# Kernel optimization log

Hardware: AMD Instinct MI355X
Metric: run time of the kernel (lower is better)

Reference implementation:

```python
import jax, jax.numpy as jnp
import numpy as np

BS, L, ED = 4, 2048, 1024
D = ED // 2          # time_embedding_dim = 512
ANG_HID = D // 4     # AngleEmb hidden = 128
T_MAX = 1010


def _gelu(x):
    return jax.nn.gelu(x, approximate=False)  # torch F.gelu default = exact erf


def _time_embed(t, w1, b1, w2, b2):
    # sinusoidal (diffusion-style, base 10000) + 2-layer MLP; t: [N] float
    half = D // 2
    freqs = jnp.exp(-jnp.log(10000.0) * jnp.arange(half, dtype=jnp.float32) / half)
    a = t[:, None] * freqs[None, :]
    e = jnp.concatenate([jnp.sin(a), jnp.cos(a)], axis=-1)  # [N, D]
    return _gelu(e @ w1 + b1) @ w2 + b2


def _cal_dist(p, aa_seq):
    # p: [bs, L, 3]; ragged per-segment mean pairwise distance.
    # Segments run (cls_idx+1 .. eos_idx-1]; token 0 = cls, token 2 = eos.
    cls = (aa_seq == 0)
    eos = (aa_seq == 2)
    seg = jnp.cumsum(cls.astype(jnp.int32), axis=1)                       # segment id
    valid = (seg > jnp.cumsum(eos.astype(jnp.int32), axis=1)) & ~cls & ~eos
    same = (seg[:, :, None] == seg[:, None, :]) & valid[:, :, None] & valid[:, None, :]
    diff = p[:, :, None, :] - p[:, None, :, :]                            # [bs,L,L,3]
    sq = jnp.sum(diff * diff, axis=-1)
    d = jnp.where(sq > 0, jnp.sqrt(jnp.where(sq > 0, sq, 1.0)), 0.0)      # safe norm
    cnt = jnp.sum(same, axis=-1)                                           # segment size (incl self)
    dist = jnp.where(valid, jnp.sum(d * same, axis=-1) / jnp.maximum(cnt, 1), 0.0)
    return dist[..., None]                                                 # [bs,L,1]


def setup_inputs() -> dict:
    key = jax.random.key(0)
    ks = jax.random.split(key, 26)
    # build ragged aa_seq: repeated [cls=0, residues in [3,25), eos=2], pad token 1
    rng = np.random.default_rng(0)
    aa = np.ones((BS, L), dtype=np.int64)
    pad = np.ones((BS, L), dtype=bool)
    for b in range(BS):
        i = 0
        while i < L - 8:
            seg = int(rng.integers(16, 64))
            seg = min(seg, L - i - 2)
            aa[b, i] = 0
            aa[b, i + 1:i + 1 + seg] = rng.integers(3, 25, size=seg)
            aa[b, i + 1 + seg] = 2
            pad[b, i:i + 2 + seg] = False
            i += seg + 2
    s = 0.05
    inp = {
        "pos": jax.random.normal(ks[0], (BS, L, 3, 3), jnp.float32) * 5.0,
        "angle": jax.random.uniform(ks[1], (BS, L, 6), jnp.float32, -3.14, 3.14),
        "padding_mask": jnp.asarray(pad),
        "mask_aa": jax.random.bernoulli(ks[2], 0.15, (BS, L, 1)),
        "mask_pos": jax.random.bernoulli(ks[3], 0.15, (BS, L, 1)),
        "mask_angle": jax.random.bernoulli(ks[4], 0.15, (BS, L, 1)),
        "angle_mask": jax.random.bernoulli(ks[5], 0.9, (BS, L, 3)),
        "bond_angle_mask": jax.random.bernoulli(ks[6], 0.9, (BS, L, 3)),
        "time_pos": jax.random.randint(ks[7], (BS, L), 0, T_MAX).astype(jnp.float32),
        "time_angle": jnp.zeros((BS, L, 6), jnp.float32),  # overwritten in fwd (dim-2 path)
        "aa_seq": jnp.asarray(aa),
        # parameters ([in, out] layout; torch Linear bias=False unless noted)
        "ang_w1": jax.random.normal(ks[8], (1, ANG_HID), jnp.float32) * 0.5,
        "ang_w2": jax.random.normal(ks[9], (ANG_HID, D), jnp.float32) * s,
        "pos_w1": jax.random.normal(ks[10], (1, 1), jnp.float32) * 0.5,
        "pos_w2": jax.random.normal(ks[11], (1, D), jnp.float32) * s,
        "te_w1": jax.random.normal(ks[12], (D, D), jnp.float32) * s,
        "te_b1": jnp.zeros((D,), jnp.float32),
        "te_w2": jax.random.normal(ks[13], (D, D), jnp.float32) * s,
        "te_b2": jnp.zeros((D,), jnp.float32),
        "angproj_w": jax.random.normal(ks[14], (6 * D, D), jnp.float32) * s,
        "angproj_b": jnp.zeros((D,), jnp.float32),
        "posproj_w": jax.random.normal(ks[15], (D, D), jnp.float32) * s,
        "posproj_b": jnp.zeros((D,), jnp.float32),
        "cls_w": jax.random.normal(ks[16], (1, ED), jnp.float32) * s,
        "eos_w": jax.random.normal(ks[17], (1, ED), jnp.float32) * s,
        "unkang_w": jax.random.normal(ks[18], (1, D), jnp.float32) * s,
        "unkpos_w": jax.random.normal(ks[19], (1, D), jnp.float32) * s,
    }
    return inp


def reference(pos, angle, padding_mask, mask_aa, mask_pos, mask_angle,
              angle_mask, bond_angle_mask, time_pos, time_angle, aa_seq,
              ang_w1, ang_w2, pos_w1, pos_w2,
              te_w1, te_b1, te_w2, te_b2,
              angproj_w, angproj_b, posproj_w, posproj_b,
              cls_w, eos_w, unkang_w, unkpos_w):
    bs, nnode, _ = angle.shape
    amask = jnp.concatenate([angle_mask[:, :, :3], bond_angle_mask], axis=-1)  # [bs,L,6]
    ang = jnp.where(amask, angle, 0.0).reshape(bs, -1, 1)                      # [bs,6L,1]
    cls_mask = (aa_seq == 0)[..., None]
    eos_mask = (aa_seq == 2)[..., None]

    angle_feat = _gelu(ang @ ang_w1) @ ang_w2                                  # [bs,6L,D]
    angle_feat = jnp.where(amask.reshape(bs, -1, 1), angle_feat, unkang_w[0])

    dist = _cal_dist(pos[:, :, 1, :], aa_seq)                                  # [bs,L,1]
    pos_feat = _gelu(dist @ pos_w1) @ pos_w2                                   # [bs,L,D]
    pos_mask = ~(cls_mask | eos_mask)
    pos_feat = jnp.where(pos_mask, pos_feat, unkpos_w[0])

    # time_pos is 2-D -> [bs,L,1]; time_angle := time_pos repeated to [bs,L,6]
    ta = jnp.where(amask, jnp.broadcast_to(time_pos[..., None], (bs, nnode, 6)), 0.0)
    temb_pos = _time_embed(time_pos.reshape(-1), te_w1, te_b1, te_w2, te_b2).reshape(bs, -1, D)
    temb_ang = _time_embed(ta.reshape(-1), te_w1, te_b1, te_w2, te_b2).reshape(bs, -1, D)
    t0_emb = _time_embed(jnp.zeros((1,), jnp.float32), te_w1, te_b1, te_w2, te_b2)[0]  # all-zero t rows are identical

    t_mask = mask_angle & ~cls_mask & ~eos_mask                                # [bs,L,1]
    temb_ang = jnp.where(jnp.tile(t_mask, (1, 6, 1)), temb_ang, t0_emb)        # torch .repeat(1,6,1)
    temb_pos = jnp.where(t_mask, temb_pos, t0_emb)
    angle_feat = angle_feat + temb_ang
    pos_feat = pos_feat + temb_pos

    angle_feat = angle_feat.reshape(bs, nnode, 6 * D) @ angproj_w + angproj_b  # [bs,L,D]
    pos_feat = pos_feat @ posproj_w + posproj_b                                # [bs,L,D]
    node = jnp.concatenate([angle_feat, pos_feat], axis=-1)                    # [bs,L,ED]
    node = jnp.where(cls_mask, cls_w[0], node)
    node = jnp.where(eos_mask, eos_w[0], node)
    node = jnp.where(padding_mask[..., None], 0.0, node)
    return node
```

## Files before the change

### kernel.cpp

```cpp
#include <hip/hip_runtime.h>
#include <hip/hip_bf16.h>
#include <cstdint>
#include <cstddef>

#define BSZ 4
#define SEQL 2048
#define DDIM 512
#define AHID 128
#define NROWS (BSZ*SEQL)
#define NANG (NROWS*6)
#define KCAT 768
#define NTT 1024

typedef __attribute__((ext_vector_type(8))) short short8;
typedef __attribute__((ext_vector_type(4))) float f32x4;
typedef __hip_bfloat16 bf16;

__device__ __forceinline__ float gelu_f(float x){
  return 0.5f * x * (1.0f + erff(x * 0.7071067811865475f));
}

__device__ __forceinline__ void gload16(const void* g, void* l){
  __builtin_amdgcn_global_load_lds(
      (const __attribute__((address_space(1))) unsigned int*)g,
      (__attribute__((address_space(3))) unsigned int*)l,
      16, 0, 0);
}

__device__ __forceinline__ unsigned int packbf2(float a, float b){
  __hip_bfloat16 ha = __float2bfloat16(a), hb = __float2bfloat16(b);
  return (unsigned int)(*(unsigned short*)&ha) | ((unsigned int)(*(unsigned short*)&hb) << 16);
}

#define NB_SCAN 4
#define NB_ANGH 3072
#define NB_SIN  256
#define NB_TR   2208
#define NB_PREP 32
#define NB_MV   224
#define NB_TOTAL (NB_SCAN+NB_ANGH+NB_SIN+NB_TR+NB_PREP+NB_MV)

__device__ void do_transpose(const float* __restrict__ W, bf16* __restrict__ Wt,
                             int K, int q, float (*tsh)[33]){
  int k0 = (q >> 4)*32, n0 = (q & 15)*32;
  int tx = threadIdx.x & 31, ty = threadIdx.x >> 5;
  #pragma unroll
  for (int i=0;i<32;i+=8)
    tsh[ty+i][tx] = W[(size_t)(k0+ty+i)*512 + n0+tx];
  __syncthreads();
  #pragma unroll
  for (int i=0;i<32;i+=8)
    Wt[(size_t)(n0+ty+i)*K + k0+tx] = __float2bfloat16(tsh[tx][ty+i]);
}

__global__ void prologue_kernel(const float* __restrict__ angle,
                                const int* __restrict__ angm, const int* __restrict__ bondm,
                                const int* __restrict__ mask_angle, const int* __restrict__ aa,
                                const int* __restrict__ padm,
                                const float* __restrict__ pos,
                                const float* __restrict__ ang_w1,
                                const float* __restrict__ te_w1, const float* __restrict__ te_w2,
                                const float* __restrict__ te_b2,
                                const float* __restrict__ ang_w2, const float* __restrict__ angproj_w,
                                const float* __restrict__ posproj_w,
                                const float* __restrict__ unkang, const float* __restrict__ pos_w2,
                                float4* __restrict__ pk,
                                bf16* __restrict__ Hang, bf16* __restrict__ et,
                                bf16* __restrict__ tw1t, bf16* __restrict__ apjt,
                                bf16* __restrict__ ppjt, bf16* __restrict__ w2b,
                                bf16* __restrict__ tw2b,
                                unsigned char* __restrict__ amb, unsigned char* __restrict__ scb,
                                float* __restrict__ U, float* __restrict__ Wg,
                                float* __restrict__ qb){
  __shared__ float tsh[32][33];
  __shared__ int wcs[4], wes[4];
  int blk = blockIdx.x;
  int tid = threadIdx.x;
  if (blk < NB_SCAN){
    int b = blk;
    int base = b*SEQL + tid*8;
    int av[8];
    int lc=0, le=0;
    #pragma unroll
    for (int i=0;i<8;i++){ int a=aa[base+i]; av[i]=a; lc += (a==0); le += (a==2); }
    int lane = tid & 63, wid = tid >> 6;
    int pc=lc, pe=le;
    #pragma unroll
    for (int off=1; off<64; off<<=1){
      int tc = __shfl_up(pc, off);
      int te = __shfl_up(pe, off);
      if (lane >= off){ pc += tc; pe += te; }
    }
    if (lane == 63){ wcs[wid] = pc; wes[wid] = pe; }
    __syncthreads();
    int c = pc - lc, eo = pe - le;
    for (int w2=0; w2<wid; w2++){ c += wcs[w2]; eo += wes[w2]; }
    #pragma unroll
    for (int i=0;i<8;i++){
      int a = av[i];
      c += (a==0); eo += (a==2);
      bool valid = (c>eo) && (a!=0) && (a!=2);
      float4 q;
      q.x = pos[(size_t)(base+i)*9+3];
      q.y = pos[(size_t)(base+i)*9+4];
      q.z = pos[(size_t)(base+i)*9+5];
      q.w = valid ? (float)c : -1.f;
      pk[base+i] = q;
    }
    return;
  }
  blk -= NB_SCAN;
  if (blk < NB_ANGH){
    int gidx = blk*256 + tid;
    int row = gidx >> 4;
    int kb = (gidx & 15) * 8;
    int bq = row / (SEQL*6);
    int rr = row - bq*(SEQL*6);
    int l = rr / 6, j = rr - l*6;
    int bl = bq*SEQL + l;
    int m = (j<3) ? angm[bl*3+j] : bondm[bl*3+(j-3)];
    float x = m ? angle[bl*6+j] : 0.f;
    float4 w0 = *(const float4*)(ang_w1+kb);
    float4 w1v = *(const float4*)(ang_w1+kb+4);
    uint4 st;
    st.x = packbf2(gelu_f(x*w0.x),  gelu_f(x*w0.y));
    st.y = packbf2(gelu_f(x*w0.z),  gelu_f(x*w0.w));
    st.z = packbf2(gelu_f(x*w1v.x), gelu_f(x*w1v.y));
    st.w = packbf2(gelu_f(x*w1v.z), gelu_f(x*w1v.w));
    *(uint4*)(Hang + (size_t)row*AHID + kb) = st;
    return;
  }
  blk -= NB_ANGH;
  if (blk < NB_SIN){
    int gidx = blk*256 + tid;
    int row = gidx >> 6;
    int db = (gidx & 63) * 8;
    float t = (float)row;
    float v[8];
    #pragma unroll
    for (int i=0;i<8;i++){
      int d = db + i;
      int k = d & 255;
      float f = exp2f(-0.05190512648262f * (float)k);
      float a = t * f;
      v[i] = (d < 256) ? __sinf(a) : __cosf(a);
    }
    uint4 st;
    st.x = packbf2(v[0],v[1]); st.y = packbf2(v[2],v[3]);
    st.z = packbf2(v[4],v[5]); st.w = packbf2(v[6],v[7]);
    *(uint4*)(et + (size_t)row*DDIM + db) = st;
    return;
  }
  blk -= NB_SIN;
  if (blk < NB_TR){
    if (blk < 256)       do_transpose(te_w1, tw1t, 512, blk, tsh);
    else if (blk < 1792) do_transpose(angproj_w, apjt, 3072, blk-256, tsh);
    else if (blk < 2048) do_transpose(posproj_w, ppjt, 512, blk-1792, tsh);
    else if (blk < 2080){
      int gidx = (blk-2048)*256 + tid;
      float4 a0 = *(const float4*)(ang_w2 + (size_t)gidx*8);
      float4 a1 = *(const float4*)(ang_w2 + (size_t)gidx*8 + 4);
      uint4 st;
      st.x = packbf2(a0.x,a0.y); st.y = packbf2(a0.z,a0.w);
      st.z = packbf2(a1.x,a1.y); st.w = packbf2(a1.z,a1.w);
      *(uint4*)(w2b + (size_t)gidx*8) = st;
    } else {
      int gidx = (blk-2080)*256 + tid;
      float4 a0 = *(const float4*)(te_w2 + (size_t)gidx*8);
      float4 a1 = *(const float4*)(te_w2 + (size_t)gidx*8 + 4);
      uint4 st;
      st.x = packbf2(a0.x,a0.y); st.y = packbf2(a0.z,a0.w);
      st.z = packbf2(a1.x,a1.y); st.w = packbf2(a1.z,a1.w);
      *(uint4*)(tw2b + (size_t)gidx*8) = st;
    }
    return;
  }
  blk -= NB_TR;
  if (blk < NB_PREP){
    int bl = blk*256 + tid;
    int b = bl >> 11, l = bl & (SEQL-1);
    int a = aa[bl];
    bool rowOK = (a!=0) && (a!=2) && (padm[bl]==0);
    int ab=0, sb=0;
    #pragma unroll
    for (int j=0;j<6;j++){
      int am = (j<3) ? angm[bl*3+j] : bondm[bl*3+(j-3)];
      int rr = l*6 + j;
      int bl2 = b*SEQL + (rr & (SEQL-1));
      int a2 = aa[bl2];
      bool tm = mask_angle[bl2] && (a2!=0) && (a2!=2);
      bool qs = tm && (am!=0) && rowOK;
      if (am)  ab |= (1<<j);
      if (qs)  sb |= (1<<j);
    }
    if ((mask_angle[bl]!=0) && rowOK) sb |= 64;
    amb[bl] = (unsigned char)ab;
    scb[bl] = (unsigned char)sb;
    return;
  }
  blk -= NB_PREP;
  {
    int q = blk;
    if (q < 96){
      int j = q >> 4, rem = q & 15;
      int nc = rem >> 3, dc = rem & 7;
      int n = nc*256 + tid, d0 = dc*64;
      float s = 0.f;
      #pragma unroll 4
      for (int i=0;i<64;i++)
        s += unkang[d0+i] * angproj_w[((size_t)(j*512 + d0+i))*512 + n];
      atomicAdd(U + j*512 + n, s);
      return;
    }
    q -= 96;
    if (q < 16){
      int nc = q >> 3, dc = q & 7;
      int n = nc*256 + tid, d0 = dc*64;
      float s = 0.f;
      #pragma unroll 4
      for (int i=0;i<64;i++)
        s += pos_w2[d0+i] * posproj_w[(size_t)(d0+i)*512 + n];
      atomicAdd(Wg + n, s);
      return;
    }
    q -= 16;
    {
      int j = q >> 4, rem = q & 15;
      int nc = rem >> 3, dc = rem & 7;
      int n = nc*256 + tid, d0 = dc*64;
      const float* W = (j<6) ? (angproj_w + (size_t)(j*512)*512) : posproj_w;
      float s = 0.f;
      #pragma unroll 4
      for (int i=0;i<64;i++)
        s += te_b2[d0+i] * W[(size_t)(d0+i)*512 + n];
      atomicAdd(qb + j*512 + n, s);
    }
  }
}

struct EpiArgs {
  const float* bias;
  const unsigned char* amb;
  const unsigned char* scb;
  const float* U;
  const float* Y;
  const float* tp;
  const int* aa;
  const int* pad;
  const float* cls;
  const float* eos;
  float* outF;
  bf16* outB;
  int cnt;
  int coloff;
  int ldc;
};

#define STG_BYTES 12288
#define SMEM_BYTES 49152

template<int EPI>
__device__ __forceinline__ void gemm_core(const char* gA, const char* gB,
                                          int K, int bm, int bn, const EpiArgs& ea, char* smem){
  const int tid = threadIdx.x;
  const int w = tid >> 6, lane = tid & 63;
  const bool doB = (w < 4);
  const int wm = (w>>1)*32, wn = (w&1)*32;
  const int lm = lane & 15, kq = lane >> 4;
  const int sw = kq ^ ((lm>>1)&3);
  const int NT = K >> 5;

  f32x4 acc[2][2];
  #pragma unroll
  for (int i=0;i<2;i++)
    #pragma unroll
    for (int j=0;j<2;j++) acc[i][j] = (f32x4){0.f,0.f,0.f,0.f};

  #pragma unroll
  for (int s=0; s<3; ++s){
    char* base = smem + s*STG_BYTES;
    gload16(gA + (size_t)s*64, base + w*1024);
    if (doB) gload16(gB + (size_t)s*64, base + 8192 + w*1024);
  }

  for (int t = 0; t < NT; ++t){
    char* cur = smem + (t&3)*STG_BYTES;
    if (t+3 < NT){
      char* nxt = smem + ((t+3)&3)*STG_BYTES;
      gload16(gA + (size_t)(t+3)*64, nxt + w*1024);
      if (doB) gload16(gB + (size_t)(t+3)*64, nxt + 8192 + w*1024);
    }
    int ia = NT-1-t; if (ia > 3) ia = 3;
    if (doB){
      if      (ia==3) __asm__ volatile("s_waitcnt vmcnt(6)" ::: "memory");
      else if (ia==2) __asm__ volatile("s_waitcnt vmcnt(4)" ::: "memory");
      else if (ia==1) __asm__ volatile("s_waitcnt vmcnt(2)" ::: "memory");
      else            __asm__ volatile("s_waitcnt vmcnt(0)" ::: "memory");
    } else {
      if      (ia==3) __asm__ volatile("s_waitcnt vmcnt(3)" ::: "memory");
      else if (ia==2) __asm__ volatile("s_waitcnt vmcnt(2)" ::: "memory");
      else if (ia==1) __asm__ volatile("s_waitcnt vmcnt(1)" ::: "memory");
      else            __asm__ volatile("s_waitcnt vmcnt(0)" ::: "memory");
    }
    __builtin_amdgcn_s_barrier();
    short8 af[2], bfr[2];
    #pragma unroll
    for (int tt=0;tt<2;tt++) af[tt]  = *(const short8*)(cur + (wm+tt*16+lm)*64 + sw*16);
    #pragma unroll
    for (int tt=0;tt<2;tt++) bfr[tt] = *(const short8*)(cur + 8192 + (wn+tt*16+lm)*64 + sw*16);
    #pragma unroll
    for (int mt=0;mt<2;mt++)
      #pragma unroll
      for (int nt=0;nt<2;nt++)
        acc[mt][nt] = __builtin_amdgcn_mfma_f32_16x16x32_bf16(af[mt], bfr[nt], acc[mt][nt], 0, 0, 0);
    __builtin_amdgcn_s_barrier();
  }

  float* eps = (float*)smem + w*576;
  const int erow = lane >> 2;
  const int ecg  = (lane & 3) * 8;
  #pragma unroll
  for (int mt=0; mt<2; mt++){
    #pragma unroll
    for (int nt=0; nt<2; nt++)
      #pragma unroll
      for (int rr=0; rr<4; rr++)
        eps[(kq*4+rr)*36 + nt*16 + lm] = acc[mt][nt][rr];
    __asm__ volatile("s_waitcnt lgkmcnt(0)" ::: "memory");
    float4 t0v = *(float4*)(eps + erow*36 + ecg);
    float4 t1v = *(float4*)(eps + erow*36 + ecg + 4);
    float v[8] = {t0v.x,t0v.y,t0v.z,t0v.w,t1v.x,t1v.y,t1v.z,t1v.w};
    __asm__ volatile("s_waitcnt lgkmcnt(0)" ::: "memory");
    int row = bm + wm + mt*16 + erow;
    int col = bn + wn + ecg;

    if (EPI==0 || EPI==1){
      float4 b0 = *(const float4*)(ea.bias+col), b1 = *(const float4*)(ea.bias+col+4);
      float bb[8] = {b0.x,b0.y,b0.z,b0.w,b1.x,b1.y,b1.z,b1.w};
      #pragma unroll
      for (int i=0;i<8;i++){
        v[i] += bb[i];
        if (EPI==0) v[i] = gelu_f(v[i]);
      }
      uint4 st;
      st.x = packbf2(v[0],v[1]); st.y = packbf2(v[2],v[3]);
      st.z = packbf2(v[4],v[5]); st.w = packbf2(v[6],v[7]);
      *(uint4*)(ea.outB + (size_t)row*ea.ldc + col) = st;
    } else if (EPI==4){
      uint4 st;
      st.x = packbf2(v[0],v[1]); st.y = packbf2(v[2],v[3]);
      st.z = packbf2(v[4],v[5]); st.w = packbf2(v[6],v[7]);
      *(uint4*)(ea.outB + (size_t)row*ea.ldc + col + ea.coloff) = st;
    } else if (EPI==5){
      float4 b0 = *(const float4*)(ea.bias+col), b1 = *(const float4*)(ea.bias+col+4);
      v[0]+=b0.x; v[1]+=b0.y; v[2]+=b0.z; v[3]+=b0.w;
      v[4]+=b1.x; v[5]+=b1.y; v[6]+=b1.z; v[7]+=b1.w;
      int ab = ea.amb[row], sc = ea.scb[row];
      int trow = (int)ea.tp[row];
      #pragma unroll
      for (int j=0;j<6;j++){
        float mU = ((ab>>j)&1) ? 0.f : 1.f;
        const float* Up = ea.U + j*512 + col;
        float4 u0=*(const float4*)Up, u1=*(const float4*)(Up+4);
        int idx = ((sc>>j)&1) ? trow : 0;
        const float* yp = ea.Y + ((size_t)j*NTT + idx)*512 + col;
        float4 y0=*(const float4*)yp, y1=*(const float4*)(yp+4);
        v[0]+=mU*u0.x+y0.x; v[1]+=mU*u0.y+y0.y;
        v[2]+=mU*u0.z+y0.z; v[3]+=mU*u0.w+y0.w;
        v[4]+=mU*u1.x+y1.x; v[5]+=mU*u1.y+y1.y;
        v[6]+=mU*u1.z+y1.z; v[7]+=mU*u1.w+y1.w;
      }
      int a = ea.aa[row];
      if (a==0){
        float4 c0 = *(const float4*)(ea.cls+col), c1 = *(const float4*)(ea.cls+col+4);
        v[0]=c0.x;v[1]=c0.y;v[2]=c0.z;v[3]=c0.w;v[4]=c1.x;v[5]=c1.y;v[6]=c1.z;v[7]=c1.w;
      } else if (a==2){
        float4 c0 = *(const float4*)(ea.eos+col), c1 = *(const float4*)(ea.eos+col+4);
        v[0]=c0.x;v[1]=c0.y;v[2]=c0.z;v[3]=c0.w;v[4]=c1.x;v[5]=c1.y;v[6]=c1.z;v[7]=c1.w;
      }
      if (ea.pad[row]){
        #pragma unroll
        for (int i=0;i<8;i++) v[i]=0.f;
      }
      *(float4*)(ea.outF + (size_t)row*ea.ldc + col)     = make_float4(v[0],v[1],v[2],v[3]);
      *(float4*)(ea.outF + (size_t)row*ea.ldc + col + 4) = make_float4(v[4],v[5],v[6],v[7]);
    } else {
      if (row < ea.cnt){
        float4 b0 = *(const float4*)(ea.bias+col), b1 = *(const float4*)(ea.bias+col+4);
        v[0]+=b0.x; v[1]+=b0.y; v[2]+=b0.z; v[3]+=b0.w;
        v[4]+=b1.x; v[5]+=b1.y; v[6]+=b1.z; v[7]+=b1.w;
        float* dst = ea.outF + (size_t)row*ea.ldc + col;
        *(float4*)dst     = make_float4(v[0],v[1],v[2],v[3]);
        *(float4*)(dst+4) = make_float4(v[4],v[5],v[6],v[7]);
      }
    }
  }
}

__device__ __forceinline__ void mk_addrs(const bf16* A, size_t lda, int bm,
                                         const bf16* Bt, size_t ldb, int bn,
                                         const char*& gA, const char*& gB){
  int tid = threadIdx.x;
  int w = tid >> 6, lane = tid & 63;
  int r = w*16 + (lane>>2);
  int cg = (lane&3) ^ ((r>>1)&3);
  gA = (const char*)(A + (size_t)(bm+r)*lda + cg*8);
  gB = (const char*)(Bt + (size_t)(bn+r)*ldb + cg*8);
}

__launch_bounds__(512, 8)
__global__ void te1_wcat_q_kernel(const bf16* __restrict__ et, const bf16* __restrict__ tw1t,
                                  EpiArgs eaH,
                                  const bf16* __restrict__ apjt, const bf16* __restrict__ ppjt,
                                  const bf16* __restrict__ w2b, const bf16* __restrict__ tw2b,
                                  EpiArgs eaW, bf16* __restrict__ QT,
                                  const float4* __restrict__ pk, float* __restrict__ dist){
  __shared__ __align__(16) char smem[SMEM_BYTES];
  int id = blockIdx.x;
  const char *gA, *gB;
  if (id < 64){
    int m = id >> 3, n = id & 7;
    mk_addrs(et, 512, m*128, tw1t, 512, n*64, gA, gB);
    gemm_core<0>(gA, gB, 512, m*128, n*64, eaH, smem);
    return;
  }
  if (id < 112){
    int q = id - 64;
    int j = q >> 3, m = (q >> 1) & 3, n = q & 1;
    mk_addrs(apjt, 3072, m*128, w2b, 512, n*64, gA, gB);
    gA += (size_t)j*512*2;
    eaW.coloff = j*128;
    gemm_core<4>(gA, gB, 512, m*128, n*64, eaW, smem);
    return;
  }
  if (id < 336){
    int q = id - 112;
    int j = q >> 5, rem = q & 31;
    int m = rem >> 3, n = rem & 7;
    if (j < 6){
      mk_addrs(apjt, 3072, m*128, tw2b, 512, n*64, gA, gB);
      gA += (size_t)j*512*2;
    } else {
      mk_addrs(ppjt, 512, m*128, tw2b, 512, n*64, gA, gB);
    }
    EpiArgs ea{};
    ea.outB = QT + (size_t)j*DDIM*DDIM; ea.ldc = DDIM; ea.coloff = 0;
    gemm_core<4>(gA, gB, 512, m*128, n*64, ea, smem);
    return;
  }
  {
    int tid = threadIdx.x;
    int gw = (id-336)*8 + (tid >> 6);
    int lane = tid & 63;
    float4 c = pk[gw];
    float out = 0.f;
    if (c.w >= 0.f){
      int rowbase = (gw >> 11) << 11;
      int jlo = gw - 64; if (jlo < rowbase) jlo = rowbase;
      int jhi = gw + 64; if (jhi >= rowbase + SEQL) jhi = rowbase + SEQL - 1;
      float s = 0.f, cnt = 0.f;
      for (int j = gw - 64 + lane; j <= jhi; j += 64){
        if (j < jlo) continue;
        float4 q = pk[j];
        if (q.w == c.w){
          float dx = c.x-q.x, dy = c.y-q.y, dz = c.z-q.z;
          float sq = dx*dx+dy*dy+dz*dz;
          s += (sq>0.f) ? sqrtf(sq) : 0.f;
          cnt += 1.f;
        }
      }
      #pragma unroll
      for (int off=32; off>0; off>>=1){
        s   += __shfl_down(s, off);
        cnt += __shfl_down(cnt, off);
      }
      out = s / fmaxf(cnt, 1.f);
    }
    if (lane==0) dist[gw] = out;
  }
}

__launch_bounds__(512, 8)
__global__ void yt_kernel(const bf16* __restrict__ H1, const bf16* __restrict__ QT,
                          const float* __restrict__ qb, float* __restrict__ YT){
  __shared__ __align__(16) char smem[SMEM_BYTES];
  int id = blockIdx.x;
  int jj = id >> 6, rem = id & 63;
  int mt = rem >> 3, nt = rem & 7;
  const char *gA, *gB;
  mk_addrs(H1, 512, mt*128, QT + (size_t)jj*DDIM*DDIM, 512, nt*64, gA, gB);
  EpiArgs ea{};
  ea.bias = qb + jj*512;
  ea.cnt = NTT;
  ea.outF = YT + (size_t)jj*NTT*512;
  ea.ldc = 512;
  gemm_core<7>(gA, gB, 512, mt*128, nt*64, ea, smem);
}

__launch_bounds__(512, 8)
__global__ void proj_kernel(const bf16* __restrict__ Hang, const bf16* __restrict__ Wcat,
                            EpiArgs eaA,
                            const int* __restrict__ aa, const int* __restrict__ padm,
                            const unsigned char* __restrict__ scb,
                            const float* __restrict__ YT,
                            const float* __restrict__ dist, const float* __restrict__ time_pos,
                            const float* __restrict__ pw1, const float* __restrict__ Wg,
                            const float* __restrict__ bp,
                            const float* __restrict__ cls, const float* __restrict__ eos,
                            float* __restrict__ out){
  __shared__ __align__(16) char smem[SMEM_BYTES];
  int id = blockIdx.x;
  if (id < 512){
    int c = id & 7, q = id >> 3;
    int n = q & 7, mh = q >> 3;
    int m = mh*8 + c;
    const char *gA, *gB;
    mk_addrs(Hang, KCAT, m*128, Wcat, KCAT, n*64, gA, gB);
    gemm_core<5>(gA, gB, KCAT, m*128, n*64, eaA, smem);
    return;
  }
  int gidx = (id-512)*512 + threadIdx.x;
  int row = gidx >> 6;
  int db = (gidx & 63) * 8;
  int a = aa[row];
  float v[8];
  if (a==0 || a==2){
    const float* src = ((a==0) ? cls : eos) + DDIM + db;
    float4 c0 = *(const float4*)src, c1 = *(const float4*)(src+4);
    v[0]=c0.x;v[1]=c0.y;v[2]=c0.z;v[3]=c0.w;v[4]=c1.x;v[5]=c1.y;v[6]=c1.z;v[7]=c1.w;
  } else {
    int sc = scb[row];
    float g = gelu_f(dist[row]*pw1[0]);
    int idx = (sc & 64) ? (int)time_pos[row] : 0;
    const float* yp = YT + ((size_t)6*NTT + idx)*512 + db;
    float4 g0 = *(const float4*)(Wg+db),  g1 = *(const float4*)(Wg+db+4);
    float4 y0 = *(const float4*)yp,       y1 = *(const float4*)(yp+4);
    float4 b0 = *(const float4*)(bp+db),  b1 = *(const float4*)(bp+db+4);
    v[0]=g*g0.x+y0.x+b0.x; v[1]=g*g0.y+y0.y+b0.y;
    v[2]=g*g0.z+y0.z+b0.z; v[3]=g*g0.w+y0.w+b0.w;
    v[4]=g*g1.x+y1.x+b1.x; v[5]=g*g1.y+y1.y+b1.y;
    v[6]=g*g1.z+y1.z+b1.z; v[7]=g*g1.w+y1.w+b1.w;
  }
  if (padm[row]){
    #pragma unroll
    for (int i=0;i<8;i++) v[i]=0.f;
  }
  float* dst = out + (size_t)row*1024 + DDIM + db;
  *(float4*)dst     = make_float4(v[0],v[1],v[2],v[3]);
  *(float4*)(dst+4) = make_float4(v[4],v[5],v[6],v[7]);
}

extern "C" void kernel_launch(void* const* d_in, const int* in_sizes, int n_in,
                              void* d_out, int out_size, void* d_ws, size_t ws_size,
                              hipStream_t stream){
  const float* pos        = (const float*)d_in[0];
  const float* angle      = (const float*)d_in[1];
  const int*   padm       = (const int*)d_in[2];
  const int*   mask_angle = (const int*)d_in[5];
  const int*   angle_mask = (const int*)d_in[6];
  const int*   bond_mask  = (const int*)d_in[7];
  const float* time_pos   = (const float*)d_in[8];
  const int*   aa         = (const int*)d_in[10];
  const float* ang_w1     = (const float*)d_in[11];
  const float* ang_w2     = (const float*)d_in[12];
  const float* pos_w1     = (const float*)d_in[13];
  const float* pos_w2     = (const float*)d_in[14];
  const float* te_w1      = (const float*)d_in[15];
  const float* te_b1      = (const float*)d_in[16];
  const float* te_w2      = (const float*)d_in[17];
  const float* te_b2      = (const float*)d_in[18];
  const float* angproj_w  = (const float*)d_in[19];
  const float* angproj_b  = (const float*)d_in[20];
  const float* posproj_w  = (const float*)d_in[21];
  const float* posproj_b  = (const float*)d_in[22];
  const float* cls_w      = (const float*)d_in[23];
  const float* eos_w      = (const float*)d_in[24];
  const float* unkang     = (const float*)d_in[25];

  char* ws = (char*)d_ws;
  size_t off = 0;
  auto alloc = [&](size_t bytes)->char*{
    char* p = ws + off;
    off += (bytes + 255) & ~(size_t)255;
    return p;
  };
  float* U      = (float*)alloc((size_t)6*DDIM*4);
  float* Wg     = (float*)alloc((size_t)DDIM*4);
  float* qb     = (float*)alloc((size_t)7*DDIM*4);
  size_t zbytes = (size_t)((char*)qb - (char*)U) + 7*DDIM*4;
  float* dist   = (float*)alloc((size_t)NROWS*4);
  float4* pk    = (float4*)alloc((size_t)NROWS*16);
  unsigned char* amb  = (unsigned char*)alloc(NROWS);
  unsigned char* scb  = (unsigned char*)alloc(NROWS);
  bf16*  et     = (bf16*) alloc((size_t)NTT*DDIM*2);
  bf16*  H1     = (bf16*) alloc((size_t)NTT*DDIM*2);
  bf16*  Hang   = (bf16*) alloc((size_t)NANG*AHID*2);
  bf16*  tw1t   = (bf16*) alloc((size_t)DDIM*DDIM*2);
  bf16*  apjt   = (bf16*) alloc((size_t)DDIM*6*DDIM*2);
  bf16*  ppjt   = (bf16*) alloc((size_t)DDIM*DDIM*2);
  bf16*  w2b    = (bf16*) alloc((size_t)AHID*DDIM*2);
  bf16*  tw2b   = (bf16*) alloc((size_t)DDIM*DDIM*2);
  bf16*  Wcat   = (bf16*) alloc((size_t)DDIM*KCAT*2);
  bf16*  QT     = (bf16*) alloc((size_t)7*DDIM*DDIM*2);
  float* YT     = (float*)alloc((size_t)7*NTT*512*4);

  float* out = (float*)d_out;
  dim3 b256(256), b512(512);

  hipMemsetAsync(U, 0, zbytes, stream);

  prologue_kernel<<<dim3(NB_TOTAL), b256, 0, stream>>>(
      angle, angle_mask, bond_mask, mask_angle, aa, padm, pos, ang_w1,
      te_w1, te_w2, te_b2, ang_w2, angproj_w, posproj_w, unkang, pos_w2,
      pk, Hang, et, tw1t, apjt, ppjt, w2b, tw2b, amb, scb, U, Wg, qb);

  EpiArgs eaH{}; eaH.bias = te_b1; eaH.outB = H1; eaH.ldc = DDIM;
  EpiArgs eaW{}; eaW.outB = Wcat; eaW.ldc = KCAT;
  te1_wcat_q_kernel<<<dim3(1360), b512, 0, stream>>>(et, tw1t, eaH,
      apjt, ppjt, w2b, tw2b, eaW, QT, pk, dist);

  yt_kernel<<<dim3(448), b512, 0, stream>>>(H1, QT, qb, YT);

  EpiArgs eaA{};
  eaA.bias = angproj_b; eaA.amb = amb; eaA.scb = scb; eaA.U = U;
  eaA.Y = YT; eaA.tp = time_pos;
  eaA.aa = aa; eaA.pad = padm; eaA.cls = cls_w; eaA.eos = eos_w;
  eaA.outF = out; eaA.ldc = 1024;
  proj_kernel<<<dim3(1536), b512, 0, stream>>>(Hang, Wcat, eaA,
      aa, padm, scb, YT, dist, time_pos, pos_w1, Wg, posproj_b, cls_w, eos_w, out);
}
```

Baseline: 179.2 us.

## Run YT and angle-projection GEMMs concurrently, move angle epilogue to separate kernel

The YT GEMM and the main angle-projection GEMM now share one launch. Before, the projection GEMM had to wait for YT because its fused epilogue read YT. The GEMM now writes a plain biased fp32 intermediate (PC). A new elementwise kernel then adds the U/YT time terms, applies the cls/eos/pad overrides, and also produces the position half. This removes the serialization between the two GEMMs and improves occupancy, at the cost of a 16 MB intermediate written and read back through global memory.

```diff
diff --git a/kernel.cpp b/kernel.cpp
--- a/kernel.cpp
+++ b/kernel.cpp
@@ -240,15 +240,6 @@
 
 struct EpiArgs {
   const float* bias;
-  const unsigned char* amb;
-  const unsigned char* scb;
-  const float* U;
-  const float* Y;
-  const float* tp;
-  const int* aa;
-  const int* pad;
-  const float* cls;
-  const float* eos;
   float* outF;
   bf16* outB;
   int cnt;
@@ -351,39 +342,6 @@
       st.x = packbf2(v[0],v[1]); st.y = packbf2(v[2],v[3]);
       st.z = packbf2(v[4],v[5]); st.w = packbf2(v[6],v[7]);
       *(uint4*)(ea.outB + (size_t)row*ea.ldc + col + ea.coloff) = st;
-    } else if (EPI==5){
-      float4 b0 = *(const float4*)(ea.bias+col), b1 = *(const float4*)(ea.bias+col+4);
-      v[0]+=b0.x; v[1]+=b0.y; v[2]+=b0.z; v[3]+=b0.w;
-      v[4]+=b1.x; v[5]+=b1.y; v[6]+=b1.z; v[7]+=b1.w;
-      int ab = ea.amb[row], sc = ea.scb[row];
-      int trow = (int)ea.tp[row];
-      #pragma unroll
-      for (int j=0;j<6;j++){
-        float mU = ((ab>>j)&1) ? 0.f : 1.f;
-        const float* Up = ea.U + j*512 + col;
-        float4 u0=*(const float4*)Up, u1=*(const float4*)(Up+4);
-        int idx = ((sc>>j)&1) ? trow : 0;
-        const float* yp = ea.Y + ((size_t)j*NTT + idx)*512 + col;
-        float4 y0=*(const float4*)yp, y1=*(const float4*)(yp+4);
-        v[0]+=mU*u0.x+y0.x; v[1]+=mU*u0.y+y0.y;
-        v[2]+=mU*u0.z+y0.z; v[3]+=mU*u0.w+y0.w;
-        v[4]+=mU*u1.x+y1.x; v[5]+=mU*u1.y+y1.y;
-        v[6]+=mU*u1.z+y1.z; v[7]+=mU*u1.w+y1.w;
-      }
-      int a = ea.aa[row];
-      if (a==0){
-        float4 c0 = *(const float4*)(ea.cls+col), c1 = *(const float4*)(ea.cls+col+4);
-        v[0]=c0.x;v[1]=c0.y;v[2]=c0.z;v[3]=c0.w;v[4]=c1.x;v[5]=c1.y;v[6]=c1.z;v[7]=c1.w;
-      } else if (a==2){
-        float4 c0 = *(const float4*)(ea.eos+col), c1 = *(const float4*)(ea.eos+col+4);
-        v[0]=c0.x;v[1]=c0.y;v[2]=c0.z;v[3]=c0.w;v[4]=c1.x;v[5]=c1.y;v[6]=c1.z;v[7]=c1.w;
-      }
-      if (ea.pad[row]){
-        #pragma unroll
-        for (int i=0;i<8;i++) v[i]=0.f;
-      }
-      *(float4*)(ea.outF + (size_t)row*ea.ldc + col)     = make_float4(v[0],v[1],v[2],v[3]);
-      *(float4*)(ea.outF + (size_t)row*ea.ldc + col + 4) = make_float4(v[4],v[5],v[6],v[7]);
     } else {
       if (row < ea.cnt){
         float4 b0 = *(const float4*)(ea.bias+col), b1 = *(const float4*)(ea.bias+col+4);
@@ -481,73 +439,121 @@
 }
 
 __launch_bounds__(512, 8)
-__global__ void yt_kernel(const bf16* __restrict__ H1, const bf16* __restrict__ QT,
-                          const float* __restrict__ qb, float* __restrict__ YT){
+__global__ void comb_kernel(const bf16* __restrict__ H1, const bf16* __restrict__ QT,
+                            const float* __restrict__ qb, float* __restrict__ YT,
+                            const bf16* __restrict__ Hang, const bf16* __restrict__ Wcat,
+                            const float* __restrict__ angproj_b, float* __restrict__ PC){
   __shared__ __align__(16) char smem[SMEM_BYTES];
   int id = blockIdx.x;
-  int jj = id >> 6, rem = id & 63;
-  int mt = rem >> 3, nt = rem & 7;
   const char *gA, *gB;
-  mk_addrs(H1, 512, mt*128, QT + (size_t)jj*DDIM*DDIM, 512, nt*64, gA, gB);
-  EpiArgs ea{};
-  ea.bias = qb + jj*512;
-  ea.cnt = NTT;
-  ea.outF = YT + (size_t)jj*NTT*512;
-  ea.ldc = 512;
-  gemm_core<7>(gA, gB, 512, mt*128, nt*64, ea, smem);
-}
-
-__launch_bounds__(512, 8)
-__global__ void proj_kernel(const bf16* __restrict__ Hang, const bf16* __restrict__ Wcat,
-                            EpiArgs eaA,
-                            const int* __restrict__ aa, const int* __restrict__ padm,
-                            const unsigned char* __restrict__ scb,
-                            const float* __restrict__ YT,
-                            const float* __restrict__ dist, const float* __restrict__ time_pos,
-                            const float* __restrict__ pw1, const float* __restrict__ Wg,
-                            const float* __restrict__ bp,
-                            const float* __restrict__ cls, const float* __restrict__ eos,
-                            float* __restrict__ out){
-  __shared__ __align__(16) char smem[SMEM_BYTES];
-  int id = blockIdx.x;
-  if (id < 512){
-    int c = id & 7, q = id >> 3;
+  if (id < 448){
+    int jj = id >> 6, rem = id & 63;
+    int mt = rem >> 3, nt = rem & 7;
+    mk_addrs(H1, 512, mt*128, QT + (size_t)jj*DDIM*DDIM, 512, nt*64, gA, gB);
+    EpiArgs ea{};
+    ea.bias = qb + jj*512;
+    ea.cnt = NTT;
+    ea.outF = YT + (size_t)jj*NTT*512;
+    ea.ldc = 512;
+    gemm_core<7>(gA, gB, 512, mt*128, nt*64, ea, smem);
+    return;
+  }
+  {
+    int id2 = id - 448;
+    int c = id2 & 7, q = id2 >> 3;
     int n = q & 7, mh = q >> 3;
     int m = mh*8 + c;
-    const char *gA, *gB;
     mk_addrs(Hang, KCAT, m*128, Wcat, KCAT, n*64, gA, gB);
-    gemm_core<5>(gA, gB, KCAT, m*128, n*64, eaA, smem);
-    return;
-  }
-  int gidx = (id-512)*512 + threadIdx.x;
-  int row = gidx >> 6;
-  int db = (gidx & 63) * 8;
-  int a = aa[row];
-  float v[8];
-  if (a==0 || a==2){
-    const float* src = ((a==0) ? cls : eos) + DDIM + db;
-    float4 c0 = *(const float4*)src, c1 = *(const float4*)(src+4);
-    v[0]=c0.x;v[1]=c0.y;v[2]=c0.z;v[3]=c0.w;v[4]=c1.x;v[5]=c1.y;v[6]=c1.z;v[7]=c1.w;
-  } else {
-    int sc = scb[row];
-    float g = gelu_f(dist[row]*pw1[0]);
-    int idx = (sc & 64) ? (int)time_pos[row] : 0;
-    const float* yp = YT + ((size_t)6*NTT + idx)*512 + db;
-    float4 g0 = *(const float4*)(Wg+db),  g1 = *(const float4*)(Wg+db+4);
-    float4 y0 = *(const float4*)yp,       y1 = *(const float4*)(yp+4);
-    float4 b0 = *(const float4*)(bp+db),  b1 = *(const float4*)(bp+db+4);
-    v[0]=g*g0.x+y0.x+b0.x; v[1]=g*g0.y+y0.y+b0.y;
-    v[2]=g*g0.z+y0.z+b0.z; v[3]=g*g0.w+y0.w+b0.w;
-    v[4]=g*g1.x+y1.x+b1.x; v[5]=g*g1.y+y1.y+b1.y;
-    v[6]=g*g1.z+y1.z+b1.z; v[7]=g*g1.w+y1.w+b1.w;
-  }
-  if (padm[row]){
-    #pragma unroll
-    for (int i=0;i<8;i++) v[i]=0.f;
-  }
-  float* dst = out + (size_t)row*1024 + DDIM + db;
-  *(float4*)dst     = make_float4(v[0],v[1],v[2],v[3]);
-  *(float4*)(dst+4) = make_float4(v[4],v[5],v[6],v[7]);
+    EpiArgs ea{};
+    ea.bias = angproj_b;
+    ea.cnt = NROWS;
+    ea.outF = PC;
+    ea.ldc = 512;
+    gemm_core<7>(gA, gB, KCAT, m*128, n*64, ea, smem);
+  }
+}
+
+__launch_bounds__(512, 8)
+__global__ void epi_kernel(const float* __restrict__ PC,
+                           const int* __restrict__ aa, const int* __restrict__ padm,
+                           const unsigned char* __restrict__ amb, const unsigned char* __restrict__ scb,
+                           const float* __restrict__ U, const float* __restrict__ YT,
+                           const float* __restrict__ dist, const float* __restrict__ time_pos,
+                           const float* __restrict__ pw1, const float* __restrict__ Wg,
+                           const float* __restrict__ bp,
+                           const float* __restrict__ cls, const float* __restrict__ eos,
+                           float* __restrict__ out){
+  int id = blockIdx.x;
+  if (id < 1024){
+    int gidx = id*512 + threadIdx.x;
+    int row = gidx >> 6;
+    int col = (gidx & 63) * 8;
+    int a = aa[row];
+    float v[8];
+    if (a==0 || a==2){
+      const float* src = ((a==0) ? cls : eos) + col;
+      float4 c0 = *(const float4*)src, c1 = *(const float4*)(src+4);
+      v[0]=c0.x;v[1]=c0.y;v[2]=c0.z;v[3]=c0.w;v[4]=c1.x;v[5]=c1.y;v[6]=c1.z;v[7]=c1.w;
+    } else {
+      const float* pc = PC + (size_t)row*512 + col;
+      float4 p0 = *(const float4*)pc, p1 = *(const float4*)(pc+4);
+      v[0]=p0.x;v[1]=p0.y;v[2]=p0.z;v[3]=p0.w;v[4]=p1.x;v[5]=p1.y;v[6]=p1.z;v[7]=p1.w;
+      int ab = amb[row], sc = scb[row];
+      int trow = (int)time_pos[row];
+      #pragma unroll
+      for (int j=0;j<6;j++){
+        float mU = ((ab>>j)&1) ? 0.f : 1.f;
+        const float* Up = U + j*512 + col;
+        float4 u0=*(const float4*)Up, u1=*(const float4*)(Up+4);
+        int idx = ((sc>>j)&1) ? trow : 0;
+        const float* yp = YT + ((size_t)j*NTT + idx)*512 + col;
+        float4 y0=*(const float4*)yp, y1=*(const float4*)(yp+4);
+        v[0]+=mU*u0.x+y0.x; v[1]+=mU*u0.y+y0.y;
+        v[2]+=mU*u0.z+y0.z; v[3]+=mU*u0.w+y0.w;
+        v[4]+=mU*u1.x+y1.x; v[5]+=mU*u1.y+y1.y;
+        v[6]+=mU*u1.z+y1.z; v[7]+=mU*u1.w+y1.w;
+      }
+    }
+    if (padm[row]){
+      #pragma unroll
+      for (int i=0;i<8;i++) v[i]=0.f;
+    }
+    float* dst = out + (size_t)row*1024 + col;
+    *(float4*)dst     = make_float4(v[0],v[1],v[2],v[3]);
+    *(float4*)(dst+4) = make_float4(v[4],v[5],v[6],v[7]);
+    return;
+  }
+  {
+    int gidx = (id-1024)*512 + threadIdx.x;
+    int row = gidx >> 6;
+    int db = (gidx & 63) * 8;
+    int a = aa[row];
+    float v[8];
+    if (a==0 || a==2){
+      const float* src = ((a==0) ? cls : eos) + DDIM + db;
+      float4 c0 = *(const float4*)src, c1 = *(const float4*)(src+4);
+      v[0]=c0.x;v[1]=c0.y;v[2]=c0.z;v[3]=c0.w;v[4]=c1.x;v[5]=c1.y;v[6]=c1.z;v[7]=c1.w;
+    } else {
+      int sc = scb[row];
+      float g = gelu_f(dist[row]*pw1[0]);
+      int idx = (sc & 64) ? (int)time_pos[row] : 0;
+      const float* yp = YT + ((size_t)6*NTT + idx)*512 + db;
+      float4 g0 = *(const float4*)(Wg+db),  g1 = *(const float4*)(Wg+db+4);
+      float4 y0 = *(const float4*)yp,       y1 = *(const float4*)(yp+4);
+      float4 b0 = *(const float4*)(bp+db),  b1 = *(const float4*)(bp+db+4);
+      v[0]=g*g0.x+y0.x+b0.x; v[1]=g*g0.y+y0.y+b0.y;
+      v[2]=g*g0.z+y0.z+b0.z; v[3]=g*g0.w+y0.w+b0.w;
+      v[4]=g*g1.x+y1.x+b1.x; v[5]=g*g1.y+y1.y+b1.y;
+      v[6]=g*g1.z+y1.z+b1.z; v[7]=g*g1.w+y1.w+b1.w;
+    }
+    if (padm[row]){
+      #pragma unroll
+      for (int i=0;i<8;i++) v[i]=0.f;
+    }
+    float* dst = out + (size_t)row*1024 + DDIM + db;
+    *(float4*)dst     = make_float4(v[0],v[1],v[2],v[3]);
+    *(float4*)(dst+4) = make_float4(v[4],v[5],v[6],v[7]);
+  }
 }
 
 extern "C" void kernel_launch(void* const* d_in, const int* in_sizes, int n_in,
@@ -603,6 +609,7 @@
   bf16*  Wcat   = (bf16*) alloc((size_t)DDIM*KCAT*2);
   bf16*  QT     = (bf16*) alloc((size_t)7*DDIM*DDIM*2);
   float* YT     = (float*)alloc((size_t)7*NTT*512*4);
+  float* PC     = (float*)alloc((size_t)NROWS*512*4);
 
   float* out = (float*)d_out;
   dim3 b256(256), b512(512);
@@ -619,13 +626,9 @@
   te1_wcat_q_kernel<<<dim3(1360), b512, 0, stream>>>(et, tw1t, eaH,
       apjt, ppjt, w2b, tw2b, eaW, QT, pk, dist);
 
-  yt_kernel<<<dim3(448), b512, 0, stream>>>(H1, QT, qb, YT);
-
-  EpiArgs eaA{};
-  eaA.bias = angproj_b; eaA.amb = amb; eaA.scb = scb; eaA.U = U;
-  eaA.Y = YT; eaA.tp = time_pos;
-  eaA.aa = aa; eaA.pad = padm; eaA.cls = cls_w; eaA.eos = eos_w;
-  eaA.outF = out; eaA.ldc = 1024;
-  proj_kernel<<<dim3(1536), b512, 0, stream>>>(Hang, Wcat, eaA,
-      aa, padm, scb, YT, dist, time_pos, pos_w1, Wg, posproj_b, cls_w, eos_w, out);
-}
+  comb_kernel<<<dim3(960), b512, 0, stream>>>(H1, QT, qb, YT,
+      Hang, Wcat, angproj_b, PC);
+
+  epi_kernel<<<dim3(2048), b512, 0, stream>>>(PC, aa, padm, amb, scb,
+      U, YT, dist, time_pos, pos_w1, Wg, posproj_b, cls_w, eos_w, out);
+}
```

New measurement: 194.4 us. 1.08x slower.
